# Optimization experiments

Measured on AMD Instinct MI355X. Metric: run time of the kernel, lower is better.

## Reference

```python
import jax, jax.numpy as jnp
import numpy as np

B, SQ, SK, D, H = 4, 2048, 2048, 1024, 16
HD = D // H
LN_EPS = 1e-5


def setup_inputs() -> dict:
    key = jax.random.key(0)
    ks = jax.random.split(key, 16)
    s = 0.02
    return {
        "query": jax.random.normal(ks[0], (B, SQ, D), jnp.float32),
        "key": jax.random.normal(ks[1], (B, SK, D), jnp.float32),
        "value": jax.random.normal(ks[2], (B, SK, D), jnp.float32),
        "attention_mask": jax.random.randint(ks[3], (B, 1, 1, SK), 0, 2, jnp.int32),
        "relative_position_bias": jax.random.normal(ks[4], (1, H, SQ, SK), jnp.float32) * s,
        "Wq": jax.random.normal(ks[5], (D, D), jnp.float32) * s,
        "bq": jnp.zeros((D,), jnp.float32),
        "Wk": jax.random.normal(ks[6], (D, D), jnp.float32) * s,
        "bk": jnp.zeros((D,), jnp.float32),
        "Wv": jax.random.normal(ks[7], (D, D), jnp.float32) * s,
        "bv": jnp.zeros((D,), jnp.float32),
        "Wo": jax.random.normal(ks[8], (D, D), jnp.float32) * s,
        "bo": jnp.zeros((D,), jnp.float32),
        "ln_gamma": jnp.ones((D,), jnp.float32),
        "ln_beta": jnp.zeros((D,), jnp.float32),
    }


def reference(query, key, value, attention_mask, relative_position_bias,
              Wq, bq, Wk, bk, Wv, bv, Wo, bo, ln_gamma, ln_beta):
    # projections (torch Linear: x @ W.T + b)
    q = query @ Wq.T + bq   # [B,Sq,D]
    k = key @ Wk.T + bk     # [B,Sk,D]
    v = value @ Wv.T + bv   # [B,Sk,D]
    # split heads -> [B,H,S,hd]
    q = q.reshape(B, SQ, H, HD).transpose(0, 2, 1, 3)
    k = k.reshape(B, SK, H, HD).transpose(0, 2, 1, 3)
    v = v.reshape(B, SK, H, HD).transpose(0, 2, 1, 3)
    scores = jnp.einsum('bhqd,bhkd->bhqk', q, k) / jnp.sqrt(jnp.float32(HD))
    scores = scores + relative_position_bias
    scores = jnp.where(attention_mask == 0, -jnp.inf, scores)
    weights = jax.nn.softmax(scores, axis=-1)  # [B,H,Sq,Sk]
    ctx = jnp.einsum('bhqk,bhkd->bhqd', weights, v)
    ctx = ctx.transpose(0, 2, 1, 3).reshape(B, SQ, D)
    out = ctx @ Wo.T + bo
    x = query + out
    mu = jnp.mean(x, axis=-1, keepdims=True)
    var = jnp.var(x, axis=-1, keepdims=True)
    return (x - mu) * jax.lax.rsqrt(var + LN_EPS) * ln_gamma + ln_beta
```

## Files before the change

### kernel.cpp

```cpp
#include <hip/hip_runtime.h>
#include <hip/hip_bf16.h>

#define B_   4
#define SQ_  2048
#define SK_  2048
#define D_   1024
#define H_   16
#define HD_  64

#define LOG2E 1.4426950408889634f

typedef __bf16 bf16_t;
typedef bf16_t bf16x8 __attribute__((ext_vector_type(8)));
typedef bf16_t bf16x4 __attribute__((ext_vector_type(4)));
typedef float  f32x4  __attribute__((ext_vector_type(4)));
typedef int    i32x4  __attribute__((ext_vector_type(4)));
typedef unsigned u32x2 __attribute__((ext_vector_type(2)));



__device__ __forceinline__ void gll16(const bf16_t* g, bf16_t* l) {
    __builtin_amdgcn_global_load_lds(
        (const __attribute__((address_space(1))) unsigned int*)g,
        (__attribute__((address_space(3))) unsigned int*)l, 16, 0, 0);
}
__device__ __forceinline__ void gll16f(const float* g, float* l) {
    __builtin_amdgcn_global_load_lds(
        (const __attribute__((address_space(1))) unsigned int*)g,
        (__attribute__((address_space(3))) unsigned int*)l, 16, 0, 0);
}

__global__ __launch_bounds__(256) void cvt_bf16(
    const float* __restrict__ p0, const float* __restrict__ p1,
    const float* __restrict__ p2, const float* __restrict__ p3,
    bf16_t* __restrict__ d, int n)
{
    int y = blockIdx.y;
    const float* s = (y == 0) ? p0 : (y == 1) ? p1 : (y == 2) ? p2 : p3;
    int i = (blockIdx.x * 256 + threadIdx.x) * 8;
    f32x4 a = *(const f32x4*)(s + i);
    f32x4 b = *(const f32x4*)(s + i + 4);
    bf16x8 o;
    #pragma unroll
    for (int j = 0; j < 4; j++) { o[j] = (bf16_t)a[j]; o[4 + j] = (bf16_t)b[j]; }
    *(bf16x8*)(d + (size_t)y * n + i) = o;
}

__global__ __launch_bounds__(256) void gemm_qkv(
    const float* __restrict__ xq, const float* __restrict__ xk, const float* __restrict__ xv,
    const bf16_t* __restrict__ wb,
    const float* __restrict__ bq, const float* __restrict__ bk, const float* __restrict__ bv,
    bf16_t* __restrict__ oq, bf16_t* __restrict__ ok, bf16_t* __restrict__ ov)
{
    __shared__ __align__(16) float  lAf[2][4096];
    __shared__ __align__(16) bf16_t lB[2][4096];

    int z = blockIdx.z;
    const float* A = (z == 0) ? xq : (z == 1) ? xk : xv;
    const bf16_t* Bm = wb + (size_t)z * 1024 * 1024;
    const float* bias = (z == 0) ? bq : (z == 1) ? bk : bv;
    bf16_t* out = (z == 0) ? oq : (z == 1) ? ok : ov;

    int tid = threadIdx.x;
    int w = tid >> 6, l = tid & 63, lr = l & 15, lg = l >> 4;
    int m0 = blockIdx.x * 128, n0 = blockIdx.y * 128;
    int wm = (w >> 1) * 64, wn = (w & 1) * 64;

    f32x4 zero4 = {0.f, 0.f, 0.f, 0.f};
    f32x4 acc[4][4];
    #pragma unroll
    for (int i = 0; i < 4; i++)
        #pragma unroll
        for (int j = 0; j < 4; j++) acc[i][j] = zero4;

    int as0 = tid, as1 = tid + 256, as2 = tid + 512, as3 = tid + 768;
    int ar0 = as0 >> 3, ar1 = as1 >> 3, ar2 = as2 >> 3, ar3 = as3 >> 3;
    const float* a_p0 = A + (size_t)(m0 + ar0) * 1024 + (((as0 & 7) ^ (ar0 & 7)) * 4);
    const float* a_p1 = A + (size_t)(m0 + ar1) * 1024 + (((as1 & 7) ^ (ar1 & 7)) * 4);
    const float* a_p2 = A + (size_t)(m0 + ar2) * 1024 + (((as2 & 7) ^ (ar2 & 7)) * 4);
    const float* a_p3 = A + (size_t)(m0 + ar3) * 1024 + (((as3 & 7) ^ (ar3 & 7)) * 4);

    int bs0 = tid, bs1 = tid + 256;
    int br0 = bs0 >> 2, br1 = bs1 >> 2;
    const bf16_t* b_p0 = Bm + (size_t)(n0 + br0) * 1024 + (((bs0 & 3) ^ ((br0 >> 1) & 3)) * 8);
    const bf16_t* b_p1 = Bm + (size_t)(n0 + br1) * 1024 + (((bs1 & 3) ^ ((br1 >> 1) & 3)) * 8);

    auto stage = [&](int buf, int kt) {
        gll16f(a_p0 + kt * 32, &lAf[buf][as0 * 4]);
        gll16f(a_p1 + kt * 32, &lAf[buf][as1 * 4]);
        gll16f(a_p2 + kt * 32, &lAf[buf][as2 * 4]);
        gll16f(a_p3 + kt * 32, &lAf[buf][as3 * 4]);
        gll16(b_p0 + kt * 32, &lB[buf][bs0 * 8]);
        gll16(b_p1 + kt * 32, &lB[buf][bs1 * 8]);
    };

    stage(0, 0);
    int buf = 0;
    #pragma unroll 1
    for (int kt = 0; kt < 32; ++kt) {
        __syncthreads();
        if (kt + 1 < 32) stage(buf ^ 1, kt + 1);
        bf16x8 af[4], bfr[4];
        #pragma unroll
        for (int i = 0; i < 4; i++) {
            int ra = wm + i * 16 + lr;
            int e = ra & 7;
            const float* arow = &lAf[buf][ra * 32];
            f32x4 lo = *(const f32x4*)(arow + ((( lg * 2)      ^ e) * 4));
            f32x4 hi = *(const f32x4*)(arow + ((((lg * 2) + 1) ^ e) * 4));
            bf16x8 a8;
            #pragma unroll
            for (int j = 0; j < 4; j++) { a8[j] = (bf16_t)lo[j]; a8[4 + j] = (bf16_t)hi[j]; }
            af[i] = a8;
            int rb = wn + i * 16 + lr;
            bfr[i] = *(const bf16x8*)&lB[buf][rb * 32 + ((lg ^ ((rb >> 1) & 3)) * 8)];
        }
        #pragma unroll
        for (int mi = 0; mi < 4; mi++)
            #pragma unroll
            for (int ni = 0; ni < 4; ni++)
                acc[mi][ni] = __builtin_amdgcn_mfma_f32_16x16x32_bf16(af[mi], bfr[ni], acc[mi][ni], 0, 0, 0);
        buf ^= 1;
    }

    #pragma unroll
    for (int mi = 0; mi < 4; mi++) {
        int row = m0 + wm + mi * 16 + lg * 4;
        int bb_ = row >> 11;
        int s   = row & 2047;
        #pragma unroll
        for (int ni = 0; ni < 4; ni++) {
            int col = n0 + wn + ni * 16 + lr;
            int hh = col >> 6, d6 = col & 63;
            float bval = bias[col];
            if (z == 0) {
                size_t obase = (((size_t)bb_ * H_ + hh) * SQ_ + s) * HD_ + d6;
                #pragma unroll
                for (int r = 0; r < 4; r++)
                    out[obase + (size_t)r * HD_] =
                        (bf16_t)((acc[mi][ni][r] + bval) * (0.125f * LOG2E));
            } else if (z == 1) {
                int kt = s >> 6, kpb = s & 63;
                size_t tb = (((size_t)bb_ * H_ + hh) * 32 + kt) * 4096;
                #pragma unroll
                for (int r = 0; r < 4; r++) {
                    int kp = kpb + r;
                    out[tb + (size_t)kp * 64 + (((d6 >> 3) ^ (kp & 7)) * 8) + (d6 & 7)] =
                        (bf16_t)(acc[mi][ni][r] + bval);
                }
            } else {
                int kt = s >> 6, kpb = s & 63;
                int chunk = ((kpb >> 5) & 1) * 4 + ((kpb >> 2) & 3);
                int jb    = ((kpb >> 4) & 1) * 4;
                size_t tb = (((size_t)bb_ * H_ + hh) * 32 + kt) * 4096;
                bf16x4 o4;
                #pragma unroll
                for (int r = 0; r < 4; r++) o4[r] = (bf16_t)(acc[mi][ni][r] + bval);
                *(bf16x4*)(out + tb + (size_t)d6 * 64 + ((chunk ^ (d6 & 7)) * 8) + jb) = o4;
            }
        }
    }
}

__global__ __launch_bounds__(256) void gemm_out(
    const bf16_t* __restrict__ A, const bf16_t* __restrict__ Bm,
    const float* __restrict__ bias, const float* __restrict__ resid,
    float* __restrict__ out)
{
    __shared__ __align__(16) bf16_t lA[2][4096];
    __shared__ __align__(16) bf16_t lB[2][4096];

    int tid = threadIdx.x;
    int w = tid >> 6, l = tid & 63, lr = l & 15, lg = l >> 4;
    int m0 = blockIdx.x * 128, n0 = blockIdx.y * 128;
    int wm = (w >> 1) * 64, wn = (w & 1) * 64;

    f32x4 zero4 = {0.f, 0.f, 0.f, 0.f};
    f32x4 acc[4][4];
    #pragma unroll
    for (int i = 0; i < 4; i++)
        #pragma unroll
        for (int j = 0; j < 4; j++) acc[i][j] = zero4;

    int s0 = tid, s1 = 256 + tid;
    int r0 = s0 >> 2, c0 = s0 & 3, r1 = s1 >> 2, c1 = s1 & 3;
    const bf16_t* a0 = A + (size_t)(m0 + r0) * 1024 + ((c0 ^ ((r0 >> 1) & 3)) * 8);
    const bf16_t* a1 = A + (size_t)(m0 + r1) * 1024 + ((c1 ^ ((r1 >> 1) & 3)) * 8);
    const bf16_t* b0 = Bm + (size_t)(n0 + r0) * 1024 + ((c0 ^ ((r0 >> 1) & 3)) * 8);
    const bf16_t* b1 = Bm + (size_t)(n0 + r1) * 1024 + ((c1 ^ ((r1 >> 1) & 3)) * 8);

    auto stage = [&](int buf, int kt) {
        gll16(a0 + kt * 32, &lA[buf][s0 * 8]);
        gll16(a1 + kt * 32, &lA[buf][s1 * 8]);
        gll16(b0 + kt * 32, &lB[buf][s0 * 8]);
        gll16(b1 + kt * 32, &lB[buf][s1 * 8]);
    };

    stage(0, 0);
    int buf = 0;
    #pragma unroll 1
    for (int kt = 0; kt < 32; ++kt) {
        __syncthreads();
        if (kt + 1 < 32) stage(buf ^ 1, kt + 1);
        bf16x8 af[4], bfr[4];
        #pragma unroll
        for (int i = 0; i < 4; i++) {
            int ra = wm + i * 16 + lr;
            af[i] = *(const bf16x8*)&lA[buf][ra * 32 + ((lg ^ ((ra >> 1) & 3)) * 8)];
            int rb = wn + i * 16 + lr;
            bfr[i] = *(const bf16x8*)&lB[buf][rb * 32 + ((lg ^ ((rb >> 1) & 3)) * 8)];
        }
        #pragma unroll
        for (int mi = 0; mi < 4; mi++)
            #pragma unroll
            for (int ni = 0; ni < 4; ni++)
                acc[mi][ni] = __builtin_amdgcn_mfma_f32_16x16x32_bf16(af[mi], bfr[ni], acc[mi][ni], 0, 0, 0);
        buf ^= 1;
    }

    #pragma unroll
    for (int mi = 0; mi < 4; mi++) {
        int row = m0 + wm + mi * 16 + lg * 4;
        #pragma unroll
        for (int ni = 0; ni < 4; ni++) {
            int col = n0 + wn + ni * 16 + lr;
            float bval = bias[col];
            #pragma unroll
            for (int r = 0; r < 4; r++) {
                size_t o = (size_t)(row + r) * D_ + col;
                out[o] = acc[mi][ni][r] + bval + resid[o];
            }
        }
    }
}

__global__ __launch_bounds__(256) void attn_kernel(
    const bf16_t* __restrict__ qg, const bf16_t* __restrict__ kgt,
    const bf16_t* __restrict__ vgt, const float* __restrict__ bias,
    const int* __restrict__ mask, bf16_t* __restrict__ ctx)
{
    __shared__ __align__(16) bf16_t ksh[2][4096];
    __shared__ __align__(16) bf16_t vsh[2][4096];
    __shared__ __align__(8) unsigned char mlds[256];

    int x = blockIdx.x;
    int g8 = x & 7;
    int rest = x >> 3;
    int b  = rest & 3;
    int tt = ((rest >> 2) << 3) | g8;
    int h  = tt >> 4;
    int qt = tt & 15;

    int tid = threadIdx.x;
    int w   = tid >> 6;
    int l   = tid & 63;
    int q16 = l & 15;
    int g   = l >> 4;
    int g4  = g * 4;

    int qrow0 = qt * 128 + w * 16 + q16;
    int qrow1 = qrow0 + 64;
    const bf16_t* qbase = qg + ((size_t)b * H_ + h) * SQ_ * HD_;
    bf16x8 qf00 = *(const bf16x8*)(qbase + (size_t)qrow0 * HD_ + g * 8);
    bf16x8 qf01 = *(const bf16x8*)(qbase + (size_t)qrow0 * HD_ + 32 + g * 8);
    bf16x8 qf10 = *(const bf16x8*)(qbase + (size_t)qrow1 * HD_ + g * 8);
    bf16x8 qf11 = *(const bf16x8*)(qbase + (size_t)qrow1 * HD_ + 32 + g * 8);

    const bf16_t* kt_base = kgt + ((size_t)b * H_ + h) * 32 * 4096;
    const bf16_t* vt_base = vgt + ((size_t)b * H_ + h) * 32 * 4096;
    const float* bias_row0 = bias + ((size_t)h * SQ_ + qrow0) * SK_;
    const float* bias_row1 = bias + ((size_t)h * SQ_ + qrow1) * SK_;

    f32x4 zero4 = {0.f, 0.f, 0.f, 0.f};
    f32x4 oacc0[4], oacc1[4];
    #pragma unroll
    for (int i = 0; i < 4; i++) { oacc0[i] = zero4; oacc1[i] = zero4; }
    f32x4 lacc0 = zero4, lacc1 = zero4;

    bf16x8 ones;
    #pragma unroll
    for (int i = 0; i < 8; i++) ones[i] = (bf16_t)1.0f;

    auto stage = [&](int buf, int t) {
        const bf16_t* ks = kt_base + (size_t)t * 4096 + tid * 8;
        const bf16_t* vs = vt_base + (size_t)t * 4096 + tid * 8;
        gll16(ks,        &ksh[buf][tid * 8]);
        gll16(ks + 2048, &ksh[buf][2048 + tid * 8]);
        gll16(vs,        &vsh[buf][tid * 8]);
        gll16(vs + 2048, &vsh[buf][2048 + tid * 8]);
    };

    stage(0, 0);
    {
        const int* mp = mask + (size_t)b * SK_ + tid * 8;
        i32x4 u0 = *(const i32x4*)mp;
        i32x4 u1 = *(const i32x4*)(mp + 4);
        unsigned by = 0;
        #pragma unroll
        for (int j = 0; j < 4; j++) by |= (u0[j] != 0 ? 1u : 0u) << j;
        #pragma unroll
        for (int j = 0; j < 4; j++) by |= (u1[j] != 0 ? 1u : 0u) << (4 + j);
        mlds[tid] = (unsigned char)by;
    }
    __syncthreads();

    #pragma unroll 1
    for (int t = 0; t < 32; ++t) {
        int buf = t & 1;
        if (t + 1 < 32) stage(buf ^ 1, t + 1);

        f32x4 bb0[4], bb1[4];
        const float* bp0 = bias_row0 + t * 64 + g4;
        const float* bp1 = bias_row1 + t * 64 + g4;
        #pragma unroll
        for (int ni = 0; ni < 4; ni++) {
            bb0[ni] = *(const f32x4*)(bp0 + ni * 16);
            bb1[ni] = *(const f32x4*)(bp1 + ni * 16);
        }
        u32x2 mm = *(const u32x2*)&mlds[t * 8];
        unsigned lo = mm[0], hi = mm[1];

        f32x4 s0[4], s1[4];
        __builtin_amdgcn_s_setprio(1);
        #pragma unroll
        for (int ni = 0; ni < 4; ni++) {
            int krow = ni * 16 + q16;
            const bf16_t* kr = &ksh[buf][0] + krow * 64;
            bf16x8 kf0 = *(const bf16x8*)(kr + ((g       ^ (krow & 7)) * 8));
            bf16x8 kf1 = *(const bf16x8*)(kr + (((4 + g) ^ (krow & 7)) * 8));
            s0[ni] = zero4; s1[ni] = zero4;
            s0[ni] = __builtin_amdgcn_mfma_f32_16x16x32_bf16(kf0, qf00, s0[ni], 0, 0, 0);
            s0[ni] = __builtin_amdgcn_mfma_f32_16x16x32_bf16(kf1, qf01, s0[ni], 0, 0, 0);
            s1[ni] = __builtin_amdgcn_mfma_f32_16x16x32_bf16(kf0, qf10, s1[ni], 0, 0, 0);
            s1[ni] = __builtin_amdgcn_mfma_f32_16x16x32_bf16(kf1, qf11, s1[ni], 0, 0, 0);
        }
        __builtin_amdgcn_s_setprio(0);

        unsigned n0_ = (lo >> g4) & 0xF;
        unsigned n1_ = (lo >> (16 + g4)) & 0xF;
        unsigned n2_ = (hi >> g4) & 0xF;
        unsigned n3_ = (hi >> (16 + g4)) & 0xF;

        bf16x8 pA0, pA1, pB0, pB1;
        #pragma unroll
        for (int r = 0; r < 4; r++) {
            float b00 = ((n0_ >> r) & 1) ? bb0[0][r] : -30000.f;
            float b01 = ((n1_ >> r) & 1) ? bb0[1][r] : -30000.f;
            float b02 = ((n2_ >> r) & 1) ? bb0[2][r] : -30000.f;
            float b03 = ((n3_ >> r) & 1) ? bb0[3][r] : -30000.f;
            pA0[r]     = (bf16_t)__builtin_amdgcn_exp2f(fmaf(b00, LOG2E, s0[0][r]));
            pA0[4 + r] = (bf16_t)__builtin_amdgcn_exp2f(fmaf(b01, LOG2E, s0[1][r]));
            pA1[r]     = (bf16_t)__builtin_amdgcn_exp2f(fmaf(b02, LOG2E, s0[2][r]));
            pA1[4 + r] = (bf16_t)__builtin_amdgcn_exp2f(fmaf(b03, LOG2E, s0[3][r]));
            float b10 = ((n0_ >> r) & 1) ? bb1[0][r] : -30000.f;
            float b11 = ((n1_ >> r) & 1) ? bb1[1][r] : -30000.f;
            float b12 = ((n2_ >> r) & 1) ? bb1[2][r] : -30000.f;
            float b13 = ((n3_ >> r) & 1) ? bb1[3][r] : -30000.f;
            pB0[r]     = (bf16_t)__builtin_amdgcn_exp2f(fmaf(b10, LOG2E, s1[0][r]));
            pB0[4 + r] = (bf16_t)__builtin_amdgcn_exp2f(fmaf(b11, LOG2E, s1[1][r]));
            pB1[r]     = (bf16_t)__builtin_amdgcn_exp2f(fmaf(b12, LOG2E, s1[2][r]));
            pB1[4 + r] = (bf16_t)__builtin_amdgcn_exp2f(fmaf(b13, LOG2E, s1[3][r]));
        }

        __builtin_amdgcn_s_setprio(1);
        lacc0 = __builtin_amdgcn_mfma_f32_16x16x32_bf16(ones, pA0, lacc0, 0, 0, 0);
        lacc0 = __builtin_amdgcn_mfma_f32_16x16x32_bf16(ones, pA1, lacc0, 0, 0, 0);
        lacc1 = __builtin_amdgcn_mfma_f32_16x16x32_bf16(ones, pB0, lacc1, 0, 0, 0);
        lacc1 = __builtin_amdgcn_mfma_f32_16x16x32_bf16(ones, pB1, lacc1, 0, 0, 0);
        #pragma unroll
        for (int nd = 0; nd < 4; nd++) {
            int vrow = nd * 16 + q16;
            const bf16_t* vr = &vsh[buf][0] + vrow * 64;
            bf16x8 vf0 = *(const bf16x8*)(vr + ((g       ^ (vrow & 7)) * 8));
            bf16x8 vf1 = *(const bf16x8*)(vr + (((4 + g) ^ (vrow & 7)) * 8));
            oacc0[nd] = __builtin_amdgcn_mfma_f32_16x16x32_bf16(vf0, pA0, oacc0[nd], 0, 0, 0);
            oacc0[nd] = __builtin_amdgcn_mfma_f32_16x16x32_bf16(vf1, pA1, oacc0[nd], 0, 0, 0);
            oacc1[nd] = __builtin_amdgcn_mfma_f32_16x16x32_bf16(vf0, pB0, oacc1[nd], 0, 0, 0);
            oacc1[nd] = __builtin_amdgcn_mfma_f32_16x16x32_bf16(vf1, pB1, oacc1[nd], 0, 0, 0);
        }
        __builtin_amdgcn_s_setprio(0);

        __syncthreads();
    }

    float l_r0 = lacc0[0];
    float l_r1 = lacc1[0];
    float inv0 = (l_r0 > 0.f) ? 1.0f / l_r0 : 0.f;
    float inv1 = (l_r1 > 0.f) ? 1.0f / l_r1 : 0.f;

    bf16_t* cp0 = ctx + ((size_t)b * SQ_ + qrow0) * D_ + (size_t)h * HD_;
    bf16_t* cp1 = ctx + ((size_t)b * SQ_ + qrow1) * D_ + (size_t)h * HD_;
    #pragma unroll
    for (int nd = 0; nd < 4; nd++) {
        bf16x4 o4, o5;
        #pragma unroll
        for (int r = 0; r < 4; r++) {
            o4[r] = (bf16_t)(oacc0[nd][r] * inv0);
            o5[r] = (bf16_t)(oacc1[nd][r] * inv1);
        }
        *(bf16x4*)(cp0 + nd * 16 + g4) = o4;
        *(bf16x4*)(cp1 + nd * 16 + g4) = o5;
    }
}

__global__ __launch_bounds__(256) void ln_kernel(
    const float* __restrict__ x, const float* __restrict__ gamma,
    const float* __restrict__ beta, float* __restrict__ out)
{
    int row = blockIdx.x;
    int t = threadIdx.x;
    const float* src = x + (size_t)row * D_;
    f32x4 v = *(const f32x4*)(src + t * 4);
    float s  = v[0] + v[1] + v[2] + v[3];
    float s2 = v[0] * v[0] + v[1] * v[1] + v[2] * v[2] + v[3] * v[3];
    #pragma unroll
    for (int off = 32; off > 0; off >>= 1) {
        s  += __shfl_down(s, off);
        s2 += __shfl_down(s2, off);
    }
    __shared__ float red[8];
    int w = t >> 6, l = t & 63;
    if (l == 0) { red[w] = s; red[4 + w] = s2; }
    __syncthreads();
    if (t == 0) {
        red[0] = red[0] + red[1] + red[2] + red[3];
        red[4] = red[4] + red[5] + red[6] + red[7];
    }
    __syncthreads();
    float mu  = red[0] * (1.0f / D_);
    float var = red[4] * (1.0f / D_) - mu * mu;
    float rstd = rsqrtf(var + 1e-5f);
    f32x4 g  = *(const f32x4*)(gamma + t * 4);
    f32x4 be = *(const f32x4*)(beta + t * 4);
    f32x4 o;
    #pragma unroll
    for (int i = 0; i < 4; i++) o[i] = (v[i] - mu) * rstd * g[i] + be[i];
    *(f32x4*)(out + (size_t)row * D_ + t * 4) = o;
}

extern "C" void kernel_launch(void* const* d_in, const int* in_sizes, int n_in,
                              void* d_out, int out_size, void* d_ws, size_t ws_size,
                              hipStream_t stream)
{
    const float* query = (const float*)d_in[0];
    const float* key   = (const float*)d_in[1];
    const float* value = (const float*)d_in[2];
    const int*   mask  = (const int*)d_in[3];
    const float* bias  = (const float*)d_in[4];
    const float* Wq    = (const float*)d_in[5];
    const float* bq    = (const float*)d_in[6];
    const float* Wk    = (const float*)d_in[7];
    const float* bk    = (const float*)d_in[8];
    const float* Wv    = (const float*)d_in[9];
    const float* bv    = (const float*)d_in[10];
    const float* Wo    = (const float*)d_in[11];
    const float* bo    = (const float*)d_in[12];
    const float* gamma = (const float*)d_in[13];
    const float* beta  = (const float*)d_in[14];
    float* out = (float*)d_out;

    char* ws = (char*)d_ws;
    const size_t MB = 1024 * 1024;
    bf16_t* ctx = (bf16_t*)(ws);
    float*  tmp = (float*)(ws + 16 * MB);
    bf16_t* wb  = (bf16_t*)(ws + 48 * MB);
    bf16_t* qb  = (bf16_t*)(ws + 56 * MB);
    bf16_t* kgt = (bf16_t*)(ws + 72 * MB);
    bf16_t* vgt = (bf16_t*)(ws + 88 * MB);

    cvt_bf16<<<dim3(512, 4), 256, 0, stream>>>(Wq, Wk, Wv, Wo, wb, 1024 * 1024);
    gemm_qkv<<<dim3(64, 8, 3), 256, 0, stream>>>(query, key, value, wb,
                                                 bq, bk, bv, qb, kgt, vgt);
    attn_kernel<<<dim3(1024), 256, 0, stream>>>(qb, kgt, vgt, bias, mask, ctx);
    gemm_out<<<dim3(64, 8), 256, 0, stream>>>(ctx, wb + (size_t)3 * 1024 * 1024, bo, query, tmp);
    ln_kernel<<<dim3(8192), 256, 0, stream>>>(tmp, gamma, beta, out);
}
```

Baseline: 325.1 us.

## Stage two K/V tiles per barrier in attention; store pre-LN residual as bf16

Result: faster. 304.9 us (-6.2%).

```diff
diff --git a/kernel.cpp b/kernel.cpp
--- a/kernel.cpp
+++ b/kernel.cpp
@@ -165,7 +165,7 @@
 __global__ __launch_bounds__(256) void gemm_out(
     const bf16_t* __restrict__ A, const bf16_t* __restrict__ Bm,
     const float* __restrict__ bias, const float* __restrict__ resid,
-    float* __restrict__ out)
+    bf16_t* __restrict__ out)
 {
     __shared__ __align__(16) bf16_t lA[2][4096];
     __shared__ __align__(16) bf16_t lB[2][4096];
@@ -228,7 +228,7 @@
             #pragma unroll
             for (int r = 0; r < 4; r++) {
                 size_t o = (size_t)(row + r) * D_ + col;
-                out[o] = acc[mi][ni][r] + bval + resid[o];
+                out[o] = (bf16_t)(acc[mi][ni][r] + bval + resid[o]);
             }
         }
     }
@@ -239,8 +239,8 @@
     const bf16_t* __restrict__ vgt, const float* __restrict__ bias,
     const int* __restrict__ mask, bf16_t* __restrict__ ctx)
 {
-    __shared__ __align__(16) bf16_t ksh[2][4096];
-    __shared__ __align__(16) bf16_t vsh[2][4096];
+    __shared__ __align__(16) bf16_t ksh[2][8192];
+    __shared__ __align__(16) bf16_t vsh[2][8192];
     __shared__ __align__(8) unsigned char mlds[256];
 
     int x = blockIdx.x;
@@ -281,34 +281,17 @@
     #pragma unroll
     for (int i = 0; i < 8; i++) ones[i] = (bf16_t)1.0f;
 
-    auto stage = [&](int buf, int t) {
-        const bf16_t* ks = kt_base + (size_t)t * 4096 + tid * 8;
-        const bf16_t* vs = vt_base + (size_t)t * 4096 + tid * 8;
-        gll16(ks,        &ksh[buf][tid * 8]);
-        gll16(ks + 2048, &ksh[buf][2048 + tid * 8]);
-        gll16(vs,        &vsh[buf][tid * 8]);
-        gll16(vs + 2048, &vsh[buf][2048 + tid * 8]);
+    auto stagePair = [&](int buf, int pt) {
+        const bf16_t* ks = kt_base + (size_t)pt * 8192 + tid * 8;
+        const bf16_t* vs = vt_base + (size_t)pt * 8192 + tid * 8;
+        #pragma unroll
+        for (int c = 0; c < 4; c++) {
+            gll16(ks + c * 2048, &ksh[buf][c * 2048 + tid * 8]);
+            gll16(vs + c * 2048, &vsh[buf][c * 2048 + tid * 8]);
+        }
     };
 
-    stage(0, 0);
-    {
-        const int* mp = mask + (size_t)b * SK_ + tid * 8;
-        i32x4 u0 = *(const i32x4*)mp;
-        i32x4 u1 = *(const i32x4*)(mp + 4);
-        unsigned by = 0;
-        #pragma unroll
-        for (int j = 0; j < 4; j++) by |= (u0[j] != 0 ? 1u : 0u) << j;
-        #pragma unroll
-        for (int j = 0; j < 4; j++) by |= (u1[j] != 0 ? 1u : 0u) << (4 + j);
-        mlds[tid] = (unsigned char)by;
-    }
-    __syncthreads();
-
-    #pragma unroll 1
-    for (int t = 0; t < 32; ++t) {
-        int buf = t & 1;
-        if (t + 1 < 32) stage(buf ^ 1, t + 1);
-
+    auto body = [&](const bf16_t* kb, const bf16_t* vb, int t) {
         f32x4 bb0[4], bb1[4];
         const float* bp0 = bias_row0 + t * 64 + g4;
         const float* bp1 = bias_row1 + t * 64 + g4;
@@ -325,7 +308,7 @@
         #pragma unroll
         for (int ni = 0; ni < 4; ni++) {
             int krow = ni * 16 + q16;
-            const bf16_t* kr = &ksh[buf][0] + krow * 64;
+            const bf16_t* kr = kb + krow * 64;
             bf16x8 kf0 = *(const bf16x8*)(kr + ((g       ^ (krow & 7)) * 8));
             bf16x8 kf1 = *(const bf16x8*)(kr + (((4 + g) ^ (krow & 7)) * 8));
             s0[ni] = zero4; s1[ni] = zero4;
@@ -370,7 +353,7 @@
         #pragma unroll
         for (int nd = 0; nd < 4; nd++) {
             int vrow = nd * 16 + q16;
-            const bf16_t* vr = &vsh[buf][0] + vrow * 64;
+            const bf16_t* vr = vb + vrow * 64;
             bf16x8 vf0 = *(const bf16x8*)(vr + ((g       ^ (vrow & 7)) * 8));
             bf16x8 vf1 = *(const bf16x8*)(vr + (((4 + g) ^ (vrow & 7)) * 8));
             oacc0[nd] = __builtin_amdgcn_mfma_f32_16x16x32_bf16(vf0, pA0, oacc0[nd], 0, 0, 0);
@@ -379,7 +362,28 @@
             oacc1[nd] = __builtin_amdgcn_mfma_f32_16x16x32_bf16(vf1, pB1, oacc1[nd], 0, 0, 0);
         }
         __builtin_amdgcn_s_setprio(0);
-
+    };
+
+    stagePair(0, 0);
+    {
+        const int* mp = mask + (size_t)b * SK_ + tid * 8;
+        i32x4 u0 = *(const i32x4*)mp;
+        i32x4 u1 = *(const i32x4*)(mp + 4);
+        unsigned by = 0;
+        #pragma unroll
+        for (int j = 0; j < 4; j++) by |= (u0[j] != 0 ? 1u : 0u) << j;
+        #pragma unroll
+        for (int j = 0; j < 4; j++) by |= (u1[j] != 0 ? 1u : 0u) << (4 + j);
+        mlds[tid] = (unsigned char)by;
+    }
+    __syncthreads();
+
+    #pragma unroll 1
+    for (int pt = 0; pt < 16; ++pt) {
+        int buf = pt & 1;
+        if (pt + 1 < 16) stagePair(buf ^ 1, pt + 1);
+        body(&ksh[buf][0],    &vsh[buf][0],    2 * pt);
+        body(&ksh[buf][4096], &vsh[buf][4096], 2 * pt + 1);
         __syncthreads();
     }
 
@@ -404,13 +408,16 @@
 }
 
 __global__ __launch_bounds__(256) void ln_kernel(
-    const float* __restrict__ x, const float* __restrict__ gamma,
+    const bf16_t* __restrict__ x, const float* __restrict__ gamma,
     const float* __restrict__ beta, float* __restrict__ out)
 {
     int row = blockIdx.x;
     int t = threadIdx.x;
-    const float* src = x + (size_t)row * D_;
-    f32x4 v = *(const f32x4*)(src + t * 4);
+    const bf16_t* src = x + (size_t)row * D_;
+    bf16x4 v4 = *(const bf16x4*)(src + t * 4);
+    f32x4 v;
+    #pragma unroll
+    for (int i = 0; i < 4; i++) v[i] = (float)v4[i];
     float s  = v[0] + v[1] + v[2] + v[3];
     float s2 = v[0] * v[0] + v[1] * v[1] + v[2] * v[2] + v[3] * v[3];
     #pragma unroll
@@ -462,7 +469,7 @@
     char* ws = (char*)d_ws;
     const size_t MB = 1024 * 1024;
     bf16_t* ctx = (bf16_t*)(ws);
-    float*  tmp = (float*)(ws + 16 * MB);
+    bf16_t* tmp = (bf16_t*)(ws + 16 * MB);
     bf16_t* wb  = (bf16_t*)(ws + 48 * MB);
     bf16_t* qb  = (bf16_t*)(ws + 56 * MB);
     bf16_t* kgt = (bf16_t*)(ws + 72 * MB);
```
